# Performance work log

Hardware: AMD Instinct MI355X
Metric: run time of the kernel (lower is better)

Reference implementation:

```python
import jax, jax.numpy as jnp
import numpy as np

B, L, D = 4, 2048, 2048
H, KVH = 16, 4
HD = D // H            # 128
G = H // KVH           # GQA group size
K_SEL = L // 4         # top_k_ratio = 0.25 -> 512
MAX_SEQ = 8192
THETA = 10000.0
SCALE = HD ** -0.5
NEG = -1e9


def _rope_tables(dim, max_len, theta):
    inv = 1.0 / theta ** (jnp.arange(0, dim, 2, dtype=jnp.float32) / dim)  # (dim/2,)
    ang = jnp.arange(max_len, dtype=jnp.float32)[:, None] * inv[None, :]   # (max_len, dim/2)
    return jnp.cos(ang), jnp.sin(ang)


def _apply_rope_pos(x, cos, sin, pos):
    # x: (B, h, K, HD), pos: (B, K) int positions
    c = cos[pos][:, None]  # (B,1,K,HD/2)
    s = sin[pos][:, None]
    x1, x2 = jnp.split(x, 2, axis=-1)
    return jnp.concatenate([x1 * c - x2 * s, x1 * s + x2 * c], axis=-1)


def setup_inputs() -> dict:
    key = jax.random.key(0)
    ks = jax.random.split(key, 8)
    std = 0.02
    x   = jax.random.normal(ks[0], (B, L, D), dtype=jnp.float32)
    Wq  = jax.random.normal(ks[1], (D, D), dtype=jnp.float32) * std
    Wkv = jax.random.normal(ks[2], (D, 2 * KVH * HD), dtype=jnp.float32) * std
    Wo  = jax.random.normal(ks[3], (D, D), dtype=jnp.float32) * std
    W1  = jax.random.normal(ks[4], (D, D // 4), dtype=jnp.float32) * std
    b1  = jnp.zeros((D // 4,), dtype=jnp.float32)
    W2  = jax.random.normal(ks[5], (D // 4, 1), dtype=jnp.float32) * std
    b2  = jnp.zeros((1,), dtype=jnp.float32)
    return {"x": x, "Wq": Wq, "Wkv": Wkv, "Wo": Wo,
            "W1": W1, "b1": b1, "W2": W2, "b2": b2}


def reference(x, Wq, Wkv, Wo, W1, b1, W2, b2):
    Bx, Lx, Dx = x.shape
    # 1. learned per-token importance scores
    imp = (jax.nn.gelu(x @ W1 + b1, approximate=False) @ W2 + b2)[..., 0]  # (B,L)
    # 2. top-k token selection, sorted to keep original order
    _, idx = jax.lax.top_k(imp, K_SEL)
    idx = jnp.sort(idx, axis=-1)                                           # (B,K)
    x_sel = jnp.take_along_axis(x, idx[..., None], axis=1)                 # (B,K,D)
    # 3. fused KV projection on the selected subset (GQA)
    kv = x_sel @ Wkv
    k, v = jnp.split(kv, 2, axis=-1)
    k = k.reshape(Bx, K_SEL, KVH, HD).transpose(0, 2, 1, 3)                # (B,KVH,K,HD)
    v = v.reshape(Bx, K_SEL, KVH, HD).transpose(0, 2, 1, 3)
    # 4. RoPE with original positions for K, contiguous positions for Q
    cos, sin = _rope_tables(HD, MAX_SEQ, THETA)
    k = _apply_rope_pos(k, cos, sin, idx)
    q = (x @ Wq).reshape(Bx, Lx, H, HD).transpose(0, 2, 1, 3)              # (B,H,L,HD)
    qpos = jnp.broadcast_to(jnp.arange(Lx)[None, :], (Bx, Lx))
    q = _apply_rope_pos(q, cos, sin, qpos)
    # 5. GQA head expansion + attention over gathered keys
    k = jnp.repeat(k, G, axis=1)                                           # (B,H,K,HD)
    v = jnp.repeat(v, G, axis=1)
    scores = jnp.einsum('bhld,bhkd->bhlk', q, k) * SCALE                   # (B,H,L,K)
    # causal mask on original key positions
    causal = idx[:, None, None, :] > jnp.arange(Lx)[None, None, :, None]
    scores = jnp.where(causal, NEG, scores)
    attn = jax.nn.softmax(scores, axis=-1)
    # 6. importance soft gating (gradient path into the scorer)
    gate = jax.nn.sigmoid(jnp.take_along_axis(imp, idx, axis=1))           # (B,K)
    attn = attn * gate[:, None, None, :]
    out = jnp.einsum('bhlk,bhkd->bhld', attn, v)                           # (B,H,L,HD)
    out = out.transpose(0, 2, 1, 3).reshape(Bx, Lx, Dx)
    return out @ Wo
```

## Files before the change

kernel.cpp:

```cpp
#include <hip/hip_runtime.h>
#include <math.h>

typedef unsigned short u16;
typedef __attribute__((ext_vector_type(8))) short short8;
typedef __attribute__((ext_vector_type(4))) float f32x4;

__device__ __forceinline__ float bf2f(u16 u) {
  return __uint_as_float(((unsigned)u) << 16);
}
__device__ __forceinline__ u16 f2bf(float f) {
  unsigned u = __float_as_uint(f);
  return (u16)((u + 0x7fffu + ((u >> 16) & 1u)) >> 16);
}

__device__ __forceinline__ void gload_lds16(const u16* g, u16* l) {
  __builtin_amdgcn_global_load_lds((const __attribute__((address_space(1))) unsigned int*)g,
                                   (__attribute__((address_space(3))) unsigned int*)l, 16, 0, 0);
}

__global__ __launch_bounds__(256) void prep_kernel(const float* __restrict__ x,
                                                   u16* __restrict__ xb,
                                                   u16* __restrict__ xlo,
                                                   const float* __restrict__ W1,
                                                   u16* __restrict__ W1Th,
                                                   u16* __restrict__ W1Tl,
                                                   const float* __restrict__ Wq,
                                                   u16* __restrict__ WqT,
                                                   const float* __restrict__ Wkv,
                                                   u16* __restrict__ WkvT,
                                                   const float* __restrict__ Wo,
                                                   u16* __restrict__ WoT,
                                                   float* __restrict__ cosT,
                                                   float* __restrict__ sinT) {
  __shared__ u16 tH[64][72];
  __shared__ u16 tL[64][72];
  int bid = blockIdx.x;
  const int t = threadIdx.x;

  if (bid < 8192) {
    size_t base = ((size_t)bid * 256 + t) * 8;
    short8 hi, lo;
    #pragma unroll
    for (int i = 0; i < 8; ++i) {
      float v = x[base + i];
      u16 h = f2bf(v);
      hi[i] = (short)h;
      lo[i] = (short)f2bf(v - bf2f(h));
    }
    *(short8*)&xb[base] = hi;
    *(short8*)&xlo[base] = lo;
    return;
  }
  bid -= 8192;

  if (bid >= 2816) {
    int gid = (bid - 2816) * 256 + t;
    int pos = gid >> 6, i = gid & 63;
    float e = (float)(2 * i) * (1.0f / 128.0f);
    float inv = powf(10000.0f, -e);
    float ang = (float)pos * inv;
    cosT[pos * 64 + i] = cosf(ang);
    sinT[pos * 64 + i] = sinf(ang);
    return;
  }

  const float* in;
  u16* oH;
  u16* oL = nullptr;
  int R, C, bx, by;
  if (bid < 256) {
    in = W1; oH = W1Th; oL = W1Tl; R = 2048; C = 512; bx = bid & 7; by = bid >> 3;
  } else if (bid < 1280) {
    bid -= 256;
    in = Wq; oH = WqT; R = 2048; C = 2048; bx = bid & 31; by = bid >> 5;
  } else if (bid < 1792) {
    bid -= 1280;
    in = Wkv; oH = WkvT; R = 2048; C = 1024; bx = bid & 15; by = bid >> 4;
  } else {
    bid -= 1792;
    in = Wo; oH = WoT; R = 2048; C = 2048; bx = bid & 31; by = bid >> 5;
  }
  int rb = by * 64, cb = bx * 64;
  #pragma unroll
  for (int i = 0; i < 16; ++i) {
    int r = i * 4 + (t >> 6), c = t & 63;
    float v = in[(size_t)(rb + r) * C + cb + c];
    u16 h = f2bf(v);
    tH[r][c] = h;
    if (oL) tL[r][c] = f2bf(v - bf2f(h));
  }
  __syncthreads();
  #pragma unroll
  for (int i = 0; i < 16; ++i) {
    int r = i * 4 + (t >> 6), c = t & 63;
    oH[(size_t)(cb + r) * R + rb + c] = tH[c][r];
    if (oL) oL[(size_t)(cb + r) * R + rb + c] = tL[c][r];
  }
}

template <bool BF16OUT>
__global__ __launch_bounds__(512, 2) void gemm256(const u16* __restrict__ A,
                                                  const u16* __restrict__ BT,
                                                  float* __restrict__ Cf,
                                                  u16* __restrict__ Cb,
                                                  int M, int N, int K) {
  __shared__ __align__(1024) u16 smem[65536];
  const int bm = blockIdx.x * 256, bn = blockIdx.y * 256;
  const int t = threadIdx.x, lane = t & 63, w = t >> 6;
  const int ll = lane & 15, lh = lane >> 4;
  const int wr = w >> 2, wc = w & 3;
  const int NT = K >> 6;

  const int tt0 = t, tt1 = t + 512;
  const int r0 = tt0 >> 2, r1 = tt1 >> 2;
  const int c0 = (((tt0 & 3) ^ ((tt0 >> 3) & 3)) << 3);
  const int c1 = (((tt1 & 3) ^ ((tt1 >> 3) & 3)) << 3);
  const size_t aoff0 = (size_t)(bm + r0) * K + c0;
  const size_t aoff1 = (size_t)(bm + r1) * K + c1;
  const size_t boff0 = (size_t)(bn + r0) * K + c0;
  const size_t boff1 = (size_t)(bn + r1) * K + c1;

  const int swz = ((lh ^ ((ll >> 1) & 3)) << 3);
  const int arow = (wr * 128 + ll) * 32 + swz;
  const int brow = (wc * 64 + ll) * 32 + swz;

  f32x4 acc[8][4];
  #pragma unroll
  for (int mi = 0; mi < 8; ++mi)
    #pragma unroll
    for (int ni = 0; ni < 4; ++ni) acc[mi][ni] = f32x4{0.f, 0.f, 0.f, 0.f};

  short8 aq[8], bq[2];

#define G_STAGE(base, o0, o1, lds) \
  gload_lds16((base) + (o0), (lds) + w * 512); \
  gload_lds16((base) + (o1), (lds) + 4096 + w * 512)
#define RD_A(Sa, ks) \
  _Pragma("unroll") for (int mi = 0; mi < 8; ++mi) aq[mi] = *(const short8*)&(Sa)[(ks)*8192 + arow + mi * 512]
#define RD_B(Sb, ks, nh) \
  _Pragma("unroll") for (int n2 = 0; n2 < 2; ++n2) bq[n2] = *(const short8*)&(Sb)[(ks)*8192 + brow + ((nh)*2 + n2) * 512]
#define DO_MFMA(nh) \
  __builtin_amdgcn_s_setprio(1); \
  _Pragma("unroll") for (int mi = 0; mi < 8; ++mi) \
    _Pragma("unroll") for (int n2 = 0; n2 < 2; ++n2) \
      acc[mi][(nh)*2 + n2] = __builtin_amdgcn_mfma_f32_16x16x32_bf16(aq[mi], bq[n2], acc[mi][(nh)*2 + n2], 0, 0, 0); \
  __builtin_amdgcn_s_setprio(0)
#define VMW(n) asm volatile("s_waitcnt vmcnt(" #n ")" ::: "memory")

  G_STAGE(A, aoff0, aoff1, smem);
  G_STAGE(BT, boff0, boff1, smem + 16384);
  G_STAGE(A, aoff0 + 32, aoff1 + 32, smem + 8192);
  G_STAGE(BT, boff0 + 32, boff1 + 32, smem + 16384 + 8192);

  for (int kt = 0; kt < NT - 1; ++kt) {
    const int cur = kt & 1;
    u16* Sa = smem + cur * 32768;
    u16* Sb = Sa + 16384;
    u16* Pa = smem + (cur ^ 1) * 32768;
    u16* Pb = Pa + 16384;
    const size_t kg = (size_t)(kt + 1) * 64;
    VMW(4);
    __builtin_amdgcn_s_barrier();
    G_STAGE(A, aoff0 + kg, aoff1 + kg, Pa);
    RD_A(Sa, 0);
    RD_B(Sb, 0, 0);
    DO_MFMA(0);
    __builtin_amdgcn_s_barrier();
    G_STAGE(BT, boff0 + kg, boff1 + kg, Pb);
    RD_B(Sb, 0, 1);
    DO_MFMA(1);
    VMW(4);
    __builtin_amdgcn_s_barrier();
    G_STAGE(A, aoff0 + kg + 32, aoff1 + kg + 32, Pa + 8192);
    RD_A(Sa, 1);
    RD_B(Sb, 1, 0);
    DO_MFMA(0);
    __builtin_amdgcn_s_barrier();
    G_STAGE(BT, boff0 + kg + 32, boff1 + kg + 32, Pb + 8192);
    RD_B(Sb, 1, 1);
    DO_MFMA(1);
  }
  {
    const int cur = (NT - 1) & 1;
    u16* Sa = smem + cur * 32768;
    u16* Sb = Sa + 16384;
    VMW(4);
    __builtin_amdgcn_s_barrier();
    RD_A(Sa, 0); RD_B(Sb, 0, 0); DO_MFMA(0);
    __builtin_amdgcn_s_barrier();
    RD_B(Sb, 0, 1); DO_MFMA(1);
    VMW(0);
    __builtin_amdgcn_s_barrier();
    RD_A(Sa, 1); RD_B(Sb, 1, 0); DO_MFMA(0);
    __builtin_amdgcn_s_barrier();
    RD_B(Sb, 1, 1); DO_MFMA(1);
  }

  #pragma unroll
  for (int mi = 0; mi < 8; ++mi)
    #pragma unroll
    for (int ni = 0; ni < 4; ++ni)
      #pragma unroll
      for (int r = 0; r < 4; ++r) {
        int row = bm + wr * 128 + mi * 16 + lh * 4 + r;
        int col = bn + wc * 64 + ni * 16 + ll;
        float v = acc[mi][ni][r];
        if (BF16OUT) Cb[(size_t)row * N + col] = f2bf(v);
        else Cf[(size_t)row * N + col] = v;
      }
#undef G_STAGE
#undef RD_A
#undef RD_B
#undef DO_MFMA
#undef VMW
}

__global__ __launch_bounds__(256) void gemm_bt_gather(const u16* __restrict__ A,
                                                      const u16* __restrict__ BT,
                                                      const int* __restrict__ rowidx,
                                                      float* __restrict__ Cpart,
                                                      int M, int N, int K) {
  __shared__ __align__(1024) u16 smem[32768];
  const int bm = blockIdx.x * 128, bn = blockIdx.y * 128;
  const int kz = blockIdx.z;
  const int t = threadIdx.x, lane = t & 63, w = t >> 6;
  const int lh = lane >> 4, ll = lane & 15;
  const int wm = (w >> 1) * 64, wn = (w & 1) * 64;

  size_t aoff[4], boff[4];
  #pragma unroll
  for (int i = 0; i < 4; ++i) {
    int c = i * 256 + t;
    int row = c >> 3;
    int gslot = (c & 7) ^ (row & 7);
    aoff[i] = (size_t)rowidx[bm + row] * K + gslot * 8;
    boff[i] = (size_t)(bn + row) * K + gslot * 8;
  }

  f32x4 acc[4][4];
  #pragma unroll
  for (int mt = 0; mt < 4; ++mt)
    #pragma unroll
    for (int nt = 0; nt < 4; ++nt) acc[mt][nt] = f32x4{0.f, 0.f, 0.f, 0.f};

#define GA_STAGE(buf, kb) \
  _Pragma("unroll") for (int i = 0; i < 4; ++i) { \
    int c = i * 256 + t; \
    gload_lds16(A + aoff[i] + (kb), (buf) + c * 8); \
    gload_lds16(BT + boff[i] + (kb), (buf) + 8192 + c * 8); \
  }
#define GVMW(n) asm volatile("s_waitcnt vmcnt(" #n ")" ::: "memory")

  const int k0 = kz * (K / 2);
  const int NT = (K / 2) / 64;

  GA_STAGE(smem, k0);

  for (int kt = 0; kt < NT; ++kt) {
    const int cur = kt & 1;
    u16* S = smem + cur * 16384;
    if (kt + 1 < NT) {
      GA_STAGE(smem + (cur ^ 1) * 16384, k0 + (kt + 1) * 64);
      GVMW(8);
    } else {
      GVMW(0);
    }
    __builtin_amdgcn_s_barrier();
    #pragma unroll
    for (int ks = 0; ks < 2; ++ks) {
      short8 a[4], b[4];
      #pragma unroll
      for (int mt = 0; mt < 4; ++mt) {
        int row = wm + mt * 16 + ll;
        int p = (ks * 4 + lh) ^ (row & 7);
        a[mt] = *(const short8*)&S[row * 64 + p * 8];
      }
      #pragma unroll
      for (int nt = 0; nt < 4; ++nt) {
        int row = wn + nt * 16 + ll;
        int p = (ks * 4 + lh) ^ (row & 7);
        b[nt] = *(const short8*)&S[8192 + row * 64 + p * 8];
      }
      __builtin_amdgcn_s_setprio(1);
      #pragma unroll
      for (int mt = 0; mt < 4; ++mt)
        #pragma unroll
        for (int nt = 0; nt < 4; ++nt)
          acc[mt][nt] = __builtin_amdgcn_mfma_f32_16x16x32_bf16(a[mt], b[nt], acc[mt][nt], 0, 0, 0);
      __builtin_amdgcn_s_setprio(0);
    }
    __builtin_amdgcn_s_barrier();
  }

  float* C = Cpart + (size_t)kz * M * N;
  #pragma unroll
  for (int mt = 0; mt < 4; ++mt)
    #pragma unroll
    for (int nt = 0; nt < 4; ++nt)
      #pragma unroll
      for (int r = 0; r < 4; ++r) {
        int row = bm + wm + mt * 16 + lh * 4 + r;
        int col = bn + wn + nt * 16 + ll;
        C[(size_t)row * N + col] = acc[mt][nt][r];
      }
#undef GA_STAGE
#undef GVMW
}

__global__ __launch_bounds__(512) void gemm_scorer(const u16* __restrict__ Ahi,
                                                   const u16* __restrict__ Alo,
                                                   const u16* __restrict__ Bhi,
                                                   const u16* __restrict__ Blo,
                                                   float* __restrict__ Cpart,
                                                   int M, int N, int K) {
  __shared__ __align__(1024) u16 smem[73728];
  const int bm = blockIdx.x * 256, bn = blockIdx.y * 128;
  const int kz = blockIdx.z;
  const int t = threadIdx.x, lane = t & 63, w = t >> 6;
  const int ll = lane & 15, lh = lane >> 4;
  const int wr = w >> 2, wc = w & 3;

  const int cA0 = (w * 2) * 64 + lane;
  const int cA1 = (w * 2 + 1) * 64 + lane;
  const int cB = w * 64 + lane;
  const size_t offA0 = (size_t)(bm + (cA0 >> 2)) * K + (((cA0 & 3) ^ ((cA0 >> 3) & 3)) << 3);
  const size_t offA1 = (size_t)(bm + (cA1 >> 2)) * K + (((cA1 & 3) ^ ((cA1 >> 3) & 3)) << 3);
  const size_t offB = (size_t)(bn + (cB >> 2)) * K + (((cB & 3) ^ ((cB >> 3) & 3)) << 3);

  const int arow = wr * 128 + ll;
  const int brow = wc * 32 + ll;

  f32x4 acc[8][2];
  #pragma unroll
  for (int mi = 0; mi < 8; ++mi)
    #pragma unroll
    for (int ni = 0; ni < 2; ++ni) acc[mi][ni] = f32x4{0.f, 0.f, 0.f, 0.f};

#define S_STAGE(buf, kb) \
  gload_lds16(Ahi + offA0 + (kb), (buf) + cA0 * 8); \
  gload_lds16(Ahi + offA1 + (kb), (buf) + cA1 * 8); \
  gload_lds16(Alo + offA0 + (kb), (buf) + 8192 + cA0 * 8); \
  gload_lds16(Alo + offA1 + (kb), (buf) + 8192 + cA1 * 8); \
  gload_lds16(Bhi + offB + (kb), (buf) + 16384 + cB * 8); \
  gload_lds16(Blo + offB + (kb), (buf) + 20480 + cB * 8)
#define SVMW(n) asm volatile("s_waitcnt vmcnt(" #n ")" ::: "memory")

  const int k0 = kz * (K / 2);
  const int NT = (K / 2) / 32;

  S_STAGE(smem, k0);
  S_STAGE(smem + 24576, k0 + 32);

  for (int kt = 0; kt < NT; ++kt) {
    u16* S = smem + (kt % 3) * 24576;
    if (kt + 1 < NT) { SVMW(6); } else { SVMW(0); }
    __builtin_amdgcn_s_barrier();
    if (kt + 2 < NT) { S_STAGE(smem + ((kt + 2) % 3) * 24576, k0 + (kt + 2) * 32); }

    short8 aH[8], aL[8], bH[2], bL[2];
    #pragma unroll
    for (int mi = 0; mi < 8; ++mi) {
      int r = arow + mi * 16;
      int o = r * 32 + ((lh ^ ((r >> 1) & 3)) << 3);
      aH[mi] = *(const short8*)&S[o];
      aL[mi] = *(const short8*)&S[8192 + o];
    }
    #pragma unroll
    for (int ni = 0; ni < 2; ++ni) {
      int r = brow + ni * 16;
      int o = r * 32 + ((lh ^ ((r >> 1) & 3)) << 3);
      bH[ni] = *(const short8*)&S[16384 + o];
      bL[ni] = *(const short8*)&S[20480 + o];
    }
    __builtin_amdgcn_s_setprio(1);
    #pragma unroll
    for (int mi = 0; mi < 8; ++mi)
      #pragma unroll
      for (int ni = 0; ni < 2; ++ni)
        acc[mi][ni] = __builtin_amdgcn_mfma_f32_16x16x32_bf16(aH[mi], bH[ni], acc[mi][ni], 0, 0, 0);
    __builtin_amdgcn_s_setprio(0);
    __builtin_amdgcn_s_setprio(1);
    #pragma unroll
    for (int mi = 0; mi < 8; ++mi)
      #pragma unroll
      for (int ni = 0; ni < 2; ++ni)
        acc[mi][ni] = __builtin_amdgcn_mfma_f32_16x16x32_bf16(aH[mi], bL[ni], acc[mi][ni], 0, 0, 0);
    __builtin_amdgcn_s_setprio(0);
    __builtin_amdgcn_s_setprio(1);
    #pragma unroll
    for (int mi = 0; mi < 8; ++mi)
      #pragma unroll
      for (int ni = 0; ni < 2; ++ni)
        acc[mi][ni] = __builtin_amdgcn_mfma_f32_16x16x32_bf16(aL[mi], bH[ni], acc[mi][ni], 0, 0, 0);
    __builtin_amdgcn_s_setprio(0);
    __builtin_amdgcn_s_barrier();
  }

  float* C = Cpart + (size_t)kz * M * N;
  #pragma unroll
  for (int mi = 0; mi < 8; ++mi)
    #pragma unroll
    for (int ni = 0; ni < 2; ++ni)
      #pragma unroll
      for (int r = 0; r < 4; ++r) {
        int row = bm + wr * 128 + mi * 16 + lh * 4 + r;
        int col = bn + wc * 32 + ni * 16 + ll;
        C[(size_t)row * N + col] = acc[mi][ni][r];
      }
#undef S_STAGE
#undef SVMW
}

__global__ __launch_bounds__(256) void scorer_finish(const float* __restrict__ hg,
                                                     const float* __restrict__ b1,
                                                     const float* __restrict__ W2,
                                                     const float* __restrict__ b2,
                                                     float* __restrict__ imp) {
  int tok = blockIdx.x * 4 + (threadIdx.x >> 6);
  int lane = threadIdx.x & 63;
  const float* h0 = hg + (size_t)tok * 512;
  const float* h1 = hg + (size_t)8192 * 512 + (size_t)tok * 512;
  float s = 0.f;
  #pragma unroll
  for (int i = 0; i < 8; ++i) {
    int c = lane + i * 64;
    float v = h0[c] + h1[c] + b1[c];
    v = 0.5f * v * (1.0f + erff(v * 0.70710678118654752f));
    s += v * W2[c];
  }
  #pragma unroll
  for (int off = 32; off; off >>= 1) s += __shfl_xor(s, off, 64);
  if (lane == 0) imp[tok] = s + b2[0];
}

__global__ __launch_bounds__(1024) void topk_kernel(const float* __restrict__ imp,
                                                    int* __restrict__ idx_sel,
                                                    int* __restrict__ sel_rows,
                                                    float* __restrict__ gatev) {
  __shared__ float v[2048];
  __shared__ int ix[2048];
  __shared__ int ids[512];
  int b = blockIdx.x, t = threadIdx.x;
  for (int i = t; i < 2048; i += 1024) { v[i] = imp[b * 2048 + i]; ix[i] = i; }
  __syncthreads();
  for (int k = 2; k <= 2048; k <<= 1)
    for (int j = k >> 1; j > 0; j >>= 1) {
      int i = ((t & ~(j - 1)) << 1) | (t & (j - 1));
      int l2 = i | j;
      bool dir = ((i & k) == 0);
      float vi = v[i], vl = v[l2];
      int xi = ix[i], xl = ix[l2];
      bool g = (vi < vl) || (vi == vl && xi > xl);
      if (g == dir) { v[i] = vl; v[l2] = vi; ix[i] = xl; ix[l2] = xi; }
      __syncthreads();
    }
  if (t < 512) ids[t] = ix[t];
  __syncthreads();
  for (int k = 2; k <= 512; k <<= 1)
    for (int j = k >> 1; j > 0; j >>= 1) {
      if (t < 256) {
        int i = ((t & ~(j - 1)) << 1) | (t & (j - 1));
        int l2 = i | j;
        bool dir = ((i & k) == 0);
        int ai = ids[i], al = ids[l2];
        if ((ai > al) == dir) { ids[i] = al; ids[l2] = ai; }
      }
      __syncthreads();
    }
  if (t < 512) {
    int id = ids[t];
    idx_sel[b * 512 + t] = id;
    sel_rows[b * 512 + t] = b * 2048 + id;
    float g = imp[b * 2048 + id];
    gatev[b * 512 + t] = 1.0f / (1.0f + __expf(-g));
  }
}

__global__ __launch_bounds__(256) void kv_finish(const float* __restrict__ part,
                                                 const int* __restrict__ idx_sel,
                                                 const float* __restrict__ cosT,
                                                 const float* __restrict__ sinT,
                                                 const float* __restrict__ gatev,
                                                 u16* __restrict__ Kb,
                                                 u16* __restrict__ VT) {
  int gid = blockIdx.x * 256 + threadIdx.x;
  if (gid < (1 << 19)) {
    int i = gid & 63;
    int s = (gid >> 6) & 511;
    int kvh = (gid >> 15) & 3;
    int b = gid >> 17;
    size_t src = (size_t)(b * 512 + s) * 1024 + kvh * 128 + i;
    float k1 = part[src] + part[src + 2097152];
    float k2 = part[src + 64] + part[src + 64 + 2097152];
    int pos = idx_sel[b * 512 + s];
    float c = cosT[pos * 64 + i], sn = sinT[pos * 64 + i];
    size_t dst = (size_t)((b * 4 + kvh) * 512 + s) * 128 + i;
    Kb[dst] = f2bf(k1 * c - k2 * sn);
    Kb[dst + 64] = f2bf(k1 * sn + k2 * c);
  } else {
    int g2 = gid - (1 << 19);
    int s = g2 & 511;
    int d = (g2 >> 9) & 127;
    int kvh = (g2 >> 16) & 3;
    int b = g2 >> 18;
    size_t src = (size_t)(b * 512 + s) * 1024 + 512 + kvh * 128 + d;
    float v = part[src] + part[src + 2097152];
    VT[(size_t)((b * 4 + kvh) * 128 + d) * 512 + s] = f2bf(v * gatev[b * 512 + s]);
  }
}

__global__ __launch_bounds__(512) void attn_kernel(const u16* __restrict__ Qb,
                                                   const u16* __restrict__ Kb,
                                                   const u16* __restrict__ VTb,
                                                   const int* __restrict__ idxp,
                                                   const float* __restrict__ cosT,
                                                   const float* __restrict__ sinT,
                                                   u16* __restrict__ Ob) {
  __shared__ u16 Ks[64][132];
  __shared__ u16 Vs[128][76];
  __shared__ u16 Ps[8][16][68];
  __shared__ int idx_s[64];

  const int qt = (blockIdx.x + 4 * blockIdx.z) & 15;
  const int h = blockIdx.y, b = blockIdx.z;
  const int kvh = h >> 2;
  const int t = threadIdx.x, lane = t & 63, w = t >> 6;
  const int lh = lane >> 4, ll = lane & 15;
  const int q0 = qt * 128;
  const float SCALE_LOG2E = 0.12753102331f;

  int NT = 8;
  if (idxp[b * 512] <= q0) {
    NT = 1;
    while (NT < 8 && idxp[b * 512 + NT * 64] <= q0 + 127) ++NT;
  }

  const int lrow = q0 + w * 16 + ll;
  short8 aq[4];
  #pragma unroll
  for (int ks = 0; ks < 4; ++ks)
    aq[ks] = *(const short8*)&Qb[(size_t)(b * 2048 + lrow) * 2048 + h * 128 + ks * 32 + lh * 8];
  {
    const float* cp = cosT + (size_t)lrow * 64 + lh * 8;
    const float* sp = sinT + (size_t)lrow * 64 + lh * 8;
    short8 n0, n1, n2, n3;
    #pragma unroll
    for (int j = 0; j < 8; ++j) {
      float cA = cp[j], sA = sp[j], cB = cp[32 + j], sB = sp[32 + j];
      float x0 = bf2f((u16)aq[0][j]), x2 = bf2f((u16)aq[2][j]);
      float x1 = bf2f((u16)aq[1][j]), x3 = bf2f((u16)aq[3][j]);
      n0[j] = (short)f2bf(x0 * cA - x2 * sA);
      n2[j] = (short)f2bf(x0 * sA + x2 * cA);
      n1[j] = (short)f2bf(x1 * cB - x3 * sB);
      n3[j] = (short)f2bf(x1 * sB + x3 * cB);
    }
    aq[0] = n0; aq[1] = n1; aq[2] = n2; aq[3] = n3;
  }

  float m[4], lden[4];
  f32x4 O[8];
  #pragma unroll
  for (int r = 0; r < 4; ++r) { m[r] = -INFINITY; lden[r] = 0.f; }
  #pragma unroll
  for (int dt = 0; dt < 8; ++dt) O[dt] = f32x4{0.f, 0.f, 0.f, 0.f};

  for (int kt = 0; kt < NT; ++kt) {
    const int tmax = idxp[b * 512 + kt * 64 + 63];
    const bool nomask = (tmax <= q0 + w * 16);

    __syncthreads();
    #pragma unroll
    for (int i = 0; i < 2; ++i) {
      int e = t + i * 512;
      int krow = e >> 4, kc8 = e & 15;
      *(short8*)&Ks[krow][kc8 * 8] =
          *(const short8*)&Kb[(size_t)((b * 4 + kvh) * 512 + kt * 64 + krow) * 128 + kc8 * 8];
      int vrow = e >> 3, vc8 = e & 7;
      *(short8*)&Vs[vrow][vc8 * 8] =
          *(const short8*)&VTb[(size_t)((b * 4 + kvh) * 128 + vrow) * 512 + kt * 64 + vc8 * 8];
    }
    if (t < 64) idx_s[t] = idxp[b * 512 + kt * 64 + t];
    __syncthreads();

    f32x4 S[4];
    #pragma unroll
    for (int nt = 0; nt < 4; ++nt) S[nt] = f32x4{0.f, 0.f, 0.f, 0.f};
    __builtin_amdgcn_s_setprio(1);
    #pragma unroll
    for (int nt = 0; nt < 4; ++nt)
      #pragma unroll
      for (int ks = 0; ks < 4; ++ks) {
        short8 bk = *(const short8*)&Ks[nt * 16 + ll][ks * 32 + lh * 8];
        S[nt] = __builtin_amdgcn_mfma_f32_16x16x32_bf16(aq[ks], bk, S[nt], 0, 0, 0);
      }
    __builtin_amdgcn_s_setprio(0);

    float p[4][4], lmax[4];
    #pragma unroll
    for (int r = 0; r < 4; ++r) lmax[r] = -INFINITY;
    if (nomask) {
      #pragma unroll
      for (int nt = 0; nt < 4; ++nt)
        #pragma unroll
        for (int r = 0; r < 4; ++r) {
          float s = S[nt][r] * SCALE_LOG2E;
          p[nt][r] = s;
          lmax[r] = fmaxf(lmax[r], s);
        }
    } else {
      #pragma unroll
      for (int nt = 0; nt < 4; ++nt) {
        int kpos = idx_s[nt * 16 + ll];
        #pragma unroll
        for (int r = 0; r < 4; ++r) {
          int row = q0 + w * 16 + lh * 4 + r;
          float s = S[nt][r] * SCALE_LOG2E;
          if (kpos > row) s = -1e9f;
          p[nt][r] = s;
          lmax[r] = fmaxf(lmax[r], s);
        }
      }
    }
    #pragma unroll
    for (int off = 8; off; off >>= 1)
      #pragma unroll
      for (int r = 0; r < 4; ++r) lmax[r] = fmaxf(lmax[r], __shfl_xor(lmax[r], off, 64));

    bool need = false;
    #pragma unroll
    for (int r = 0; r < 4; ++r) need = need || (lmax[r] > m[r] + 8.0f);
    if (__any(need)) {
      #pragma unroll
      for (int r = 0; r < 4; ++r) {
        float mnew = fmaxf(m[r], lmax[r]);
        float alpha = exp2f(m[r] - mnew);
        m[r] = mnew;
        lden[r] *= alpha;
        #pragma unroll
        for (int dt = 0; dt < 8; ++dt) O[dt][r] *= alpha;
      }
    }

    float rs[4] = {0.f, 0.f, 0.f, 0.f};
    #pragma unroll
    for (int nt = 0; nt < 4; ++nt)
      #pragma unroll
      for (int r = 0; r < 4; ++r) {
        float e = exp2f(p[nt][r] - m[r]);
        p[nt][r] = e;
        rs[r] += e;
      }
    #pragma unroll
    for (int off = 8; off; off >>= 1)
      #pragma unroll
      for (int r = 0; r < 4; ++r) rs[r] += __shfl_xor(rs[r], off, 64);
    #pragma unroll
    for (int r = 0; r < 4; ++r) lden[r] += rs[r];

    #pragma unroll
    for (int nt = 0; nt < 4; ++nt)
      #pragma unroll
      for (int r = 0; r < 4; r += 2) {
        unsigned pk;
        asm("v_cvt_pk_bf16_f32 %0, %1, %2" : "=v"(pk) : "v"(p[nt][r]), "v"(p[nt][r + 1]));
        Ps[w][lh * 4 + r][nt * 16 + ll] = (u16)pk;
        Ps[w][lh * 4 + r + 1][nt * 16 + ll] = (u16)(pk >> 16);
      }
    __builtin_amdgcn_s_setprio(1);
    #pragma unroll
    for (int ks = 0; ks < 2; ++ks) {
      short8 pa = *(const short8*)&Ps[w][ll][ks * 32 + lh * 8];
      #pragma unroll
      for (int dt = 0; dt < 8; ++dt) {
        short8 vb = *(const short8*)&Vs[dt * 16 + ll][ks * 32 + lh * 8];
        O[dt] = __builtin_amdgcn_mfma_f32_16x16x32_bf16(pa, vb, O[dt], 0, 0, 0);
      }
    }
    __builtin_amdgcn_s_setprio(0);
  }

  #pragma unroll
  for (int dt = 0; dt < 8; ++dt)
    #pragma unroll
    for (int r = 0; r < 4; ++r) {
      int row = q0 + w * 16 + lh * 4 + r;
      int col = h * 128 + dt * 16 + ll;
      Ob[(size_t)(b * 2048 + row) * 2048 + col] = f2bf(O[dt][r] / lden[r]);
    }
}

extern "C" void kernel_launch(void* const* d_in, const int* in_sizes, int n_in,
                              void* d_out, int out_size, void* d_ws, size_t ws_size,
                              hipStream_t stream) {
  const float* x = (const float*)d_in[0];
  const float* Wq = (const float*)d_in[1];
  const float* Wkv = (const float*)d_in[2];
  const float* Wo = (const float*)d_in[3];
  const float* W1 = (const float*)d_in[4];
  const float* b1 = (const float*)d_in[5];
  const float* W2 = (const float*)d_in[6];
  const float* b2 = (const float*)d_in[7];
  float* out = (float*)d_out;

  char* ws = (char*)d_ws;
  size_t off = 0;
  auto alloc = [&](size_t bytes) {
    char* p = ws + off;
    off = (off + bytes + 255) & ~(size_t)255;
    return p;
  };
  u16* xb = (u16*)alloc((size_t)8192 * 2048 * 2);
  u16* xlo = (u16*)alloc((size_t)8192 * 2048 * 2);
  u16* W1Th = (u16*)alloc((size_t)512 * 2048 * 2);
  u16* W1Tl = (u16*)alloc((size_t)512 * 2048 * 2);
  u16* WqT = (u16*)alloc((size_t)2048 * 2048 * 2);
  u16* WkvT = (u16*)alloc((size_t)1024 * 2048 * 2);
  u16* WoT = (u16*)alloc((size_t)2048 * 2048 * 2);
  float* cosT = (float*)alloc((size_t)2048 * 64 * 4);
  float* sinT = (float*)alloc((size_t)2048 * 64 * 4);
  float* hg = (float*)alloc((size_t)2 * 8192 * 512 * 4);
  float* impv = (float*)alloc((size_t)8192 * 4);
  int* idx_sel = (int*)alloc((size_t)2048 * 4);
  int* sel_rows = (int*)alloc((size_t)2048 * 4);
  float* gatev = (float*)alloc((size_t)2048 * 4);
  u16* qbuf = (u16*)alloc((size_t)8192 * 2048 * 2);
  u16* Kbuf = (u16*)alloc((size_t)4 * 4 * 512 * 128 * 2);
  u16* VTbuf = (u16*)alloc((size_t)4 * 4 * 128 * 512 * 2);
  u16* attn_out = xlo;
  float* kvpart = hg;

  prep_kernel<<<11520, 256, 0, stream>>>(x, xb, xlo, W1, W1Th, W1Tl, Wq, WqT,
                                         Wkv, WkvT, Wo, WoT, cosT, sinT);

  gemm_scorer<<<dim3(32, 4, 2), 512, 0, stream>>>(xb, xlo, W1Th, W1Tl, hg, 8192, 512, 2048);
  scorer_finish<<<2048, 256, 0, stream>>>(hg, b1, W2, b2, impv);
  topk_kernel<<<4, 1024, 0, stream>>>(impv, idx_sel, sel_rows, gatev);

  gemm256<true><<<dim3(32, 8), 512, 0, stream>>>(xb, WqT, nullptr, qbuf, 8192, 2048, 2048);

  gemm_bt_gather<<<dim3(16, 8, 2), 256, 0, stream>>>(xb, WkvT, sel_rows, kvpart, 2048, 1024, 2048);
  kv_finish<<<6144, 256, 0, stream>>>(kvpart, idx_sel, cosT, sinT, gatev, Kbuf, VTbuf);

  attn_kernel<<<dim3(16, 16, 4), 512, 0, stream>>>(qbuf, Kbuf, VTbuf, idx_sel, cosT, sinT, attn_out);

  gemm256<false><<<dim3(32, 8), 512, 0, stream>>>(attn_out, WoT, out, nullptr, 8192, 2048, 2048);
}
```

Measured before the change: 376.4 us.

## Replace bitonic sort top-k with radix select and prefix-sum compaction

The top-k kernel previously bitonic-sorted all 2048 importance scores and then bitonic-sorted the 512 selected indices, which costs many barrier-separated passes. It now maps floats to order-preserving unsigned keys and runs a 4-pass 8-bit radix select to find the k-th threshold key. A block-wide prefix scan then compacts the selected indices in original order, breaking ties by lowest index. This needs far fewer synchronization steps, but relies on shared-memory atomics and a packed 16-bit counter scan.

```diff
diff --git a/kernel.cpp b/kernel.cpp
--- a/kernel.cpp
+++ b/kernel.cpp
@@ -437,42 +437,89 @@
                                                     int* __restrict__ idx_sel,
                                                     int* __restrict__ sel_rows,
                                                     float* __restrict__ gatev) {
-  __shared__ float v[2048];
-  __shared__ int ix[2048];
-  __shared__ int ids[512];
-  int b = blockIdx.x, t = threadIdx.x;
-  for (int i = t; i < 2048; i += 1024) { v[i] = imp[b * 2048 + i]; ix[i] = i; }
+  __shared__ unsigned key[2048];
+  __shared__ unsigned suff[256];
+  __shared__ unsigned ps[1024];
+  __shared__ unsigned sh_known, sh_need;
+  const int b = blockIdx.x, t = threadIdx.x;
+  const int lane = t & 63;
+
+  for (int i = t; i < 2048; i += 1024) {
+    unsigned u = __float_as_uint(imp[b * 2048 + i]);
+    key[i] = u ^ ((u & 0x80000000u) ? 0xFFFFFFFFu : 0x80000000u);
+  }
+  if (t == 0) { sh_known = 0u; sh_need = 512u; }
   __syncthreads();
-  for (int k = 2; k <= 2048; k <<= 1)
-    for (int j = k >> 1; j > 0; j >>= 1) {
-      int i = ((t & ~(j - 1)) << 1) | (t & (j - 1));
-      int l2 = i | j;
-      bool dir = ((i & k) == 0);
-      float vi = v[i], vl = v[l2];
-      int xi = ix[i], xl = ix[l2];
-      bool g = (vi < vl) || (vi == vl && xi > xl);
-      if (g == dir) { v[i] = vl; v[l2] = vi; ix[i] = xl; ix[l2] = xi; }
-      __syncthreads();
-    }
-  if (t < 512) ids[t] = ix[t];
+
+  unsigned kmask = 0u;
+  #pragma unroll
+  for (int shift = 24; shift >= 0; shift -= 8) {
+    unsigned known = sh_known;
+    if (t < 256) suff[t] = 0u;
+    __syncthreads();
+    for (int i = t; i < 2048; i += 1024)
+      if ((key[i] & kmask) == known) atomicAdd(&suff[(key[i] >> shift) & 255], 1u);
+    __syncthreads();
+    if (t < 64) {
+      unsigned cbin0 = suff[4 * lane], cbin1 = suff[4 * lane + 1];
+      unsigned cbin2 = suff[4 * lane + 2], cbin3 = suff[4 * lane + 3];
+      unsigned s = cbin0 + cbin1 + cbin2 + cbin3;
+      unsigned acc = s;
+      #pragma unroll
+      for (int off = 1; off < 64; off <<= 1) {
+        unsigned tmp = __shfl_down(acc, off, 64);
+        if (lane + off < 64) acc += tmp;
+      }
+      unsigned sfx = acc - s;
+      suff[4 * lane + 3] = sfx + cbin3;
+      suff[4 * lane + 2] = sfx + cbin3 + cbin2;
+      suff[4 * lane + 1] = sfx + cbin3 + cbin2 + cbin1;
+      suff[4 * lane]     = sfx + cbin3 + cbin2 + cbin1 + cbin0;
+    }
+    __syncthreads();
+    unsigned need = sh_need;
+    if (t < 256) {
+      unsigned above = (t == 255) ? 0u : suff[t + 1];
+      if (suff[t] >= need && above < need) {
+        sh_known = known | ((unsigned)t << shift);
+        sh_need = need - above;
+      }
+    }
+    __syncthreads();
+    kmask |= (255u << shift);
+  }
+
+  const unsigned Kstar = sh_known;
+  const unsigned need = sh_need;
+
+  unsigned k0 = key[2 * t], k1 = key[2 * t + 1];
+  unsigned a0 = ((k0 == Kstar) ? 0x10000u : 0u) | ((k0 > Kstar) ? 1u : 0u);
+  unsigned a1 = ((k1 == Kstar) ? 0x10000u : 0u) | ((k1 > Kstar) ? 1u : 0u);
+  ps[t] = a0 + a1;
   __syncthreads();
-  for (int k = 2; k <= 512; k <<= 1)
-    for (int j = k >> 1; j > 0; j >>= 1) {
-      if (t < 256) {
-        int i = ((t & ~(j - 1)) << 1) | (t & (j - 1));
-        int l2 = i | j;
-        bool dir = ((i & k) == 0);
-        int ai = ids[i], al = ids[l2];
-        if ((ai > al) == dir) { ids[i] = al; ids[l2] = ai; }
-      }
-      __syncthreads();
-    }
-  if (t < 512) {
-    int id = ids[t];
-    idx_sel[b * 512 + t] = id;
-    sel_rows[b * 512 + t] = b * 2048 + id;
-    float g = imp[b * 2048 + id];
-    gatev[b * 512 + t] = 1.0f / (1.0f + __expf(-g));
+  for (int off = 1; off < 1024; off <<= 1) {
+    unsigned add = (t >= off) ? ps[t - off] : 0u;
+    __syncthreads();
+    ps[t] += add;
+    __syncthreads();
+  }
+  unsigned ex0 = (t == 0) ? 0u : ps[t - 1];
+  unsigned ex1 = ex0 + a0;
+
+  #pragma unroll
+  for (int e = 0; e < 2; ++e) {
+    int i = 2 * t + e;
+    unsigned k = e ? k1 : k0;
+    unsigned ex = e ? ex1 : ex0;
+    unsigned eqr = ex >> 16, gtc = ex & 0xFFFFu;
+    bool sel = (k > Kstar) || ((k == Kstar) && eqr < need);
+    if (sel) {
+      unsigned pos = gtc + ((eqr < need) ? eqr : need);
+      idx_sel[b * 512 + pos] = i;
+      sel_rows[b * 512 + pos] = b * 2048 + i;
+      float g = imp[b * 2048 + i];
+      gatev[b * 512 + pos] = 1.0f / (1.0f + __expf(-g));
+    }
   }
 }
 
```

Measured after the change: 356.8 us. 5.2% less time.
